# Kernel optimization log

Hardware: AMD Instinct MI355X
Metric: run time of the kernel (lower is better)

The kernel has to match this reference:

```python
import jax, jax.numpy as jnp
import numpy as np

COST_CLASS, COST_BBOX, COST_GIOU = 1.0, 5.0, 2.0


def box_cxcywh_to_xyxy(b):
    cx, cy, w, h = jnp.split(b, 4, axis=-1)
    return jnp.concatenate([cx - 0.5 * w, cy - 0.5 * h, cx + 0.5 * w, cy + 0.5 * h], axis=-1)


def generalized_box_iou(a, b):
    # a: [N,4], b: [T,4] in xyxy -> [N,T]
    area_a = (a[:, 2] - a[:, 0]) * (a[:, 3] - a[:, 1])
    area_b = (b[:, 2] - b[:, 0]) * (b[:, 3] - b[:, 1])
    lt = jnp.maximum(a[:, None, :2], b[None, :, :2])
    rb = jnp.minimum(a[:, None, 2:], b[None, :, 2:])
    wh = jnp.clip(rb - lt, 0.0)
    inter = wh[..., 0] * wh[..., 1]
    union = area_a[:, None] + area_b[None, :] - inter
    iou = inter / union
    lt_e = jnp.minimum(a[:, None, :2], b[None, :, :2])
    rb_e = jnp.maximum(a[:, None, 2:], b[None, :, 2:])
    wh_e = jnp.clip(rb_e - lt_e, 0.0)
    area_e = wh_e[..., 0] * wh_e[..., 1]
    return iou - (area_e - union) / area_e


def cost_matrix(pred_logits, pred_boxes, tgt_labels, tgt_boxes):
    B, Q, _ = pred_logits.shape
    probs = jax.nn.softmax(pred_logits.reshape(B * Q, -1), axis=-1)
    pb = pred_boxes.reshape(B * Q, 4)
    tl = tgt_labels.reshape(-1)
    tb = tgt_boxes.reshape(-1, 4)
    cc = -probs[:, tl]                                              # [BQ, BM]
    cb = jnp.sum(jnp.abs(pb[:, None, :] - tb[None, :, :]), axis=-1)  # L1 cdist
    cg = -generalized_box_iou(box_cxcywh_to_xyxy(pb), box_cxcywh_to_xyxy(tb))
    C = COST_CLASS * cc + COST_BBOX * cb + COST_GIOU * cg
    return C.reshape(B, Q, -1)


def hungarian(cost):
    # Jonker-Volgenant shortest-augmenting-path assignment.
    # cost: [n, m] with n <= m; returns the column assigned to each row, [n] int32.
    n, m = cost.shape
    INF = jnp.float32(1e30)

    def solve_row(i, uvp):
        u, v, p = uvp  # u:[n+1] row potentials (+dummy), v:[m+1], p:[m+1] row assigned per col
        p = p.at[m].set(i)  # virtual start column m holds the new row
        state = (jnp.int32(m), u, v, p,
                 jnp.full(m + 1, INF, jnp.float32),   # minv
                 jnp.zeros(m + 1, bool),              # used
                 jnp.zeros(m + 1, jnp.int32))         # way

        def cond(s):
            j0, _, _, p, _, _, _ = s
            return p[j0] != -1

        def body(s):
            j0, u, v, p, minv, used, way = s
            used = used.at[j0].set(True)
            i0 = p[j0]
            cur = jnp.where(used[:m], INF, cost[i0] - u[i0] - v[:m])
            better = cur < minv[:m]
            minv = minv.at[:m].set(jnp.where(better, cur, minv[:m]))
            way = way.at[:m].set(jnp.where(better, j0, way[:m]))
            masked = jnp.where(used[:m], INF, minv[:m])
            j1 = jnp.argmin(masked).astype(jnp.int32)
            delta = masked[j1]
            u = u.at[jnp.where(used, p, n)].add(jnp.where(used, delta, 0.0))
            v = jnp.where(used, v - delta, v)
            minv = jnp.where(used, minv, minv - delta)
            return (j1, u, v, p, minv, used, way)

        j0, u, v, p, minv, used, way = jax.lax.while_loop(cond, body, state)

        def a_cond(s):
            return s[0] != m

        def a_body(s):
            j0, p = s
            j1 = way[j0]
            return (j1, p.at[j0].set(p[j1]))

        _, p = jax.lax.while_loop(a_cond, a_body, (j0, p))
        return (u, v, p)

    u0 = jnp.zeros(n + 1, jnp.float32)
    v0 = jnp.zeros(m + 1, jnp.float32)
    p0 = jnp.full(m + 1, -1, jnp.int32)
    _, _, p = jax.lax.fori_loop(0, n, solve_row, (u0, v0, p0))
    row_of_col = p[:m]
    cols = jnp.arange(m, dtype=jnp.int32)
    col_of_row = jnp.zeros(n + 1, jnp.int32).at[
        jnp.where(row_of_col >= 0, row_of_col, n)].set(cols)
    return col_of_row[:n]


def setup_inputs() -> dict:
    key = jax.random.key(0)
    k1, k2, k3, k4 = jax.random.split(key, 4)
    B, Q, NCLS, M = 32, 300, 92, 50
    return {
        'pred_logits': jax.random.normal(k1, (B, Q, NCLS), jnp.float32),
        'pred_boxes': jax.random.uniform(k2, (B, Q, 4), dtype=jnp.float32),
        'tgt_labels': jax.random.randint(k3, (B, M), 0, NCLS),
        'tgt_boxes': jax.random.uniform(k4, (B, M, 4), dtype=jnp.float32),
    }


def reference(pred_logits, pred_boxes, tgt_labels, tgt_boxes):
    B, Q, _ = pred_logits.shape
    M = tgt_labels.shape[1]
    C = cost_matrix(pred_logits, pred_boxes, tgt_labels, tgt_boxes)  # [B, Q, B*M]
    # per-image block of columns: C[i, :, i*M:(i+1)*M]
    C4 = C.reshape(B, Q, B, M)
    C_per = jnp.transpose(jnp.diagonal(C4, axis1=0, axis2=2), (2, 0, 1))  # [B, Q, M]
    q = jax.vmap(hungarian)(jnp.transpose(C_per, (0, 2, 1)))  # [B, M]: query per target
    order = jnp.argsort(q, axis=1).astype(jnp.int32)
    pred_idx = jnp.take_along_axis(q, order, axis=1)  # sorted query indices
    gt_idx = order                                     # matching target indices
    return pred_idx, gt_idx, C
```

## Files before the change

kernel.cpp:

```cpp
#include <hip/hip_runtime.h>

#define NB   32
#define NQ   300
#define NCLS 92
#define NM   50
#define BM   (NB * NM)
#define BQ   (NB * NQ)
#define HM   NQ
#define HN   NM
#define PITCH 305
#define BIG  1e30f
#define HUNG_BLOCKS NB
#define COST_ROWS_PER_BLOCK 16
#define COST_BLOCKS (BQ / COST_ROWS_PER_BLOCK)
#define NBLOCKS (HUNG_BLOCKS + COST_BLOCKS)

typedef float vf4 __attribute__((ext_vector_type(4)));

#define FENCE() __threadfence_block()

#define DPP_XOR1  0xB1
#define DPP_XOR2  0x4E
#define DPP_HMIRR 0x141
#define DPP_MIRR  0x140
#define DPP_BC15  0x142
#define DPP_BC31  0x143

template <int C_>
__device__ __forceinline__ float dppk(float v) {
  return __int_as_float(__builtin_amdgcn_update_dpp(
      __float_as_int(v), __float_as_int(v), C_, 0xf, 0xf, false));
}
template <int C_>
__device__ __forceinline__ float dppz(float v) {
  return __int_as_float(
      __builtin_amdgcn_update_dpp(0, __float_as_int(v), C_, 0xf, 0xf, true));
}

__device__ __forceinline__ float rl63(float v) {
  return __int_as_float(__builtin_amdgcn_readlane(__float_as_int(v), 63));
}
__device__ __forceinline__ int rli(int v, int l) {
  return __builtin_amdgcn_readlane(v, l);
}
__device__ __forceinline__ float rlf(float v, int l) {
  return __int_as_float(__builtin_amdgcn_readlane(__float_as_int(v), l));
}

__device__ __forceinline__ float wredu_max(float v) {
  v = fmaxf(v, dppk<DPP_XOR1>(v));
  v = fmaxf(v, dppk<DPP_XOR2>(v));
  v = fmaxf(v, dppk<DPP_HMIRR>(v));
  v = fmaxf(v, dppk<DPP_MIRR>(v));
  v = fmaxf(v, dppk<DPP_BC15>(v));
  v = fmaxf(v, dppk<DPP_BC31>(v));
  return rl63(v);
}
__device__ __forceinline__ float wredu_min(float v) {
  v = fminf(v, dppk<DPP_XOR1>(v));
  v = fminf(v, dppk<DPP_XOR2>(v));
  v = fminf(v, dppk<DPP_HMIRR>(v));
  v = fminf(v, dppk<DPP_MIRR>(v));
  v = fminf(v, dppk<DPP_BC15>(v));
  v = fminf(v, dppk<DPP_BC31>(v));
  return rl63(v);
}
__device__ __forceinline__ float wredu_sum(float v) {
  v += dppz<DPP_XOR1>(v);
  v += dppz<DPP_XOR2>(v);
  v += dppz<DPP_HMIRR>(v);
  v += dppz<DPP_MIRR>(v);
  v += dppz<DPP_BC15>(v);
  v += dppz<DPP_BC31>(v);
  return rl63(v);
}

__device__ __forceinline__ float pair_cost(float ax1, float ay1, float ax2,
                                           float ay2, float areaA,
                                           const float4& pb, const float4& t,
                                           float negprob) {
  float cb = fabsf(pb.x - t.x) + fabsf(pb.y - t.y) +
             fabsf(pb.z - t.z) + fabsf(pb.w - t.w);
  float bx1 = t.x - 0.5f * t.z, by1 = t.y - 0.5f * t.w;
  float bx2 = t.x + 0.5f * t.z, by2 = t.y + 0.5f * t.w;
  float areaB = (bx2 - bx1) * (by2 - by1);
  float iw = fmaxf(fminf(ax2, bx2) - fmaxf(ax1, bx1), 0.f);
  float ih = fmaxf(fminf(ay2, by2) - fmaxf(ay1, by1), 0.f);
  float inter = iw * ih;
  float uni = areaA + areaB - inter;
  float iou = inter / uni;
  float ew = fmaxf(fmaxf(ax2, bx2) - fminf(ax1, bx1), 0.f);
  float eh = fmaxf(fmaxf(ay2, by2) - fminf(ay1, by1), 0.f);
  float areaE = ew * eh;
  float giou = iou - (areaE - uni) / areaE;
  return (negprob + 5.f * cb) - 2.f * giou;
}

__device__ __forceinline__ void wave_softmax(const float* __restrict__ lrow,
                                             float* prow, int lane) {
  float x0 = lrow[lane];
  float x1 = (lane + 64 < NCLS) ? lrow[lane + 64] : -BIG;
  float mx = wredu_max(fmaxf(x0, x1));
  float e0 = expf(x0 - mx), e1 = expf(x1 - mx);
  float s = wredu_sum(e0 + e1);
  prow[lane] = e0 / s;
  if (lane + 64 < NCLS) prow[lane + 64] = e1 / s;
  FENCE();
}

__global__ __launch_bounds__(1024) void fused_kernel(
    const float* __restrict__ logits, const float* __restrict__ pboxes,
    const int* __restrict__ tlab, const float* __restrict__ tbox,
    float* __restrict__ outp) {
  __shared__ float hc[HN * PITCH];
  __shared__ float probs_s[16][NCLS];
  __shared__ int   p[HM + 1];
  __shared__ int   way[HM];
  __shared__ int   qarr[HN];

  float* C = outp + 2 * BM;
  int tid = threadIdx.x, wave = tid >> 6, lane = tid & 63;

  if (blockIdx.x >= HUNG_BLOCKS) {
    int row = (blockIdx.x - HUNG_BLOCKS) * COST_ROWS_PER_BLOCK + wave;
    wave_softmax(logits + (size_t)row * NCLS, probs_s[wave], lane);

    float4 pb = reinterpret_cast<const float4*>(pboxes)[row];
    float ax1 = pb.x - 0.5f * pb.z, ay1 = pb.y - 0.5f * pb.w;
    float ax2 = pb.x + 0.5f * pb.z, ay2 = pb.y + 0.5f * pb.w;
    float areaA = (ax2 - ax1) * (ay2 - ay1);

    const float4* tbv = reinterpret_cast<const float4*>(tbox);
    const int4*   tlv = reinterpret_cast<const int4*>(tlab);
    vf4* crow = reinterpret_cast<vf4*>(C + (size_t)row * BM);
    for (int q4 = lane; q4 < BM / 4; q4 += 64) {
      int4 cls = tlv[q4];
      int clsa[4] = {cls.x, cls.y, cls.z, cls.w};
      vf4 o;
#pragma unroll
      for (int e = 0; e < 4; e++) {
        float4 t = tbv[q4 * 4 + e];
        o[e] = pair_cost(ax1, ay1, ax2, ay2, areaA, pb, t,
                         -probs_s[wave][clsa[e]]);
      }
      __builtin_nontemporal_store(o, &crow[q4]);
    }
    return;
  }

  int b = blockIdx.x;

  for (int x = tid; x <= HM; x += 1024) p[x] = -1;

  float4 t_reg = make_float4(0.f, 0.f, 0.f, 0.f);
  int cls_reg = 0;
  if (lane < NM) {
    t_reg = reinterpret_cast<const float4*>(tbox)[b * NM + lane];
    cls_reg = tlab[b * NM + lane];
  }

  const float4* pbv = reinterpret_cast<const float4*>(pboxes);
  for (int q = wave; q < NQ; q += 16) {
    const float* lrow = logits + (size_t)(b * NQ + q) * NCLS;
    float x0 = lrow[lane];
    float x1 = (lane + 64 < NCLS) ? lrow[lane + 64] : -BIG;
    float mx = wredu_max(fmaxf(x0, x1));
    float e0 = expf(x0 - mx), e1 = expf(x1 - mx);
    float s = wredu_sum(e0 + e1);
    float g0 = __shfl(x0, cls_reg, 64);
    float g1 = __shfl(x1, cls_reg, 64);
    float xsel = (cls_reg < 64) ? g0 : g1;
    float negp = -(expf(xsel - mx) / s);

    float4 pb = pbv[b * NQ + q];
    float ax1 = pb.x - 0.5f * pb.z, ay1 = pb.y - 0.5f * pb.w;
    float ax2 = pb.x + 0.5f * pb.z, ay2 = pb.y + 0.5f * pb.w;
    float areaA = (ax2 - ax1) * (ay2 - ay1);
    if (lane < NM) {
      hc[lane * PITCH + q] =
          pair_cost(ax1, ay1, ax2, ay2, areaA, pb, t_reg, negp);
    }
  }
  __syncthreads();
  if (wave != 0) return;


  float u_reg = 0.f;
  int am_reg = 0;
  if (lane < HN) {
    const float* r = &hc[lane * PITCH];
    float mn0 = BIG, mn1 = BIG;
    int a0 = 0, a1 = 1;
    for (int j = 0; j < HM; j += 2) {
      float va = r[j], vb = r[j + 1];
      if (va < mn0) { mn0 = va; a0 = j; }
      if (vb < mn1) { mn1 = vb; a1 = j + 1; }
    }
    bool takeOdd = (mn1 < mn0) || (mn1 == mn0 && a1 < a0);
    u_reg = takeOdd ? mn1 : mn0;
    am_reg = takeOdd ? a1 : a0;
  }

  unsigned amask = 0;
  unsigned long long pending = 0;
  for (int i = 0; i < HN; i++) {
    int jm = rli(am_reg, i);
    unsigned mrem = (unsigned)rli((int)amask, jm & 63);
    if (!((mrem >> (jm >> 6)) & 1u)) {
      if (lane == (jm & 63)) amask |= 1u << (jm >> 6);
      if (lane == 0) p[jm] = i;
    } else {
      pending |= 1ull << i;
    }
  }
  FENCE();

  float v_r[5], minv_r[5];
#pragma unroll
  for (int k = 0; k < 5; k++) v_r[k] = 0.f;

  while (pending) {
    int i_start = (int)__ffsll((long long)pending) - 1;
    pending &= pending - 1;
#pragma unroll
    for (int k = 0; k < 5; k++) minv_r[k] = BIG;
    unsigned usedc = 0;
    unsigned long long used_rows = 1ull << i_start;
    int i0 = i_start, j0 = HM, jfree = -1;
    float ui0 = rlf(u_reg, i0);

    while (true) {
      float best = BIG; int bj = 0;
      const float* hrow = &hc[i0 * PITCH];
#pragma unroll
      for (int k = 0; k < 5; k++) {
        int j = lane + 64 * k;
        if (j < HM && !((usedc >> k) & 1u)) {
          float cur = hrow[j] - ui0 - v_r[k];
          if (cur < minv_r[k]) { minv_r[k] = cur; way[j] = j0; }
          if (minv_r[k] < best) { best = minv_r[k]; bj = j; }
        }
      }
      float wmin = wredu_min(best);
      unsigned long long ball = __ballot(best == wmin);
      int src = (int)__ffsll((long long)ball) - 1;
      int j1 = rli(bj, src);
      float delta = wmin;

      int psel = p[j1];

      if ((used_rows >> lane) & 1ull) u_reg += delta;
#pragma unroll
      for (int k = 0; k < 5; k++) {
        int j = lane + 64 * k;
        if (j < HM) {
          if ((usedc >> k) & 1u) v_r[k] -= delta;
          else                   minv_r[k] -= delta;
        }
      }
      if (lane == (j1 & 63)) usedc |= 1u << (j1 >> 6);

      if (psel == -1) { jfree = j1; break; }
      i0 = psel;
      used_rows |= 1ull << i0;
      ui0 = rlf(u_reg, i0);
      j0 = j1;
    }

    int jj = jfree;
    while (jj != HM) {
      int jn = way[jj];
      int pv = (jn == HM) ? i_start : p[jn];
      p[jj] = pv;
      jj = jn;
    }
    FENCE();
  }

  for (int j = lane; j < HM; j += 64) {
    int r = p[j];
    if (r >= 0) qarr[r] = j;
  }
  FENCE();
  if (lane < HN) {
    int qi = qarr[lane];
    int rank = 0;
    for (int t = 0; t < HN; t++) rank += (qarr[t] < qi);
    outp[(size_t)b * NM + rank] = (float)qi;
    outp[BM + (size_t)b * NM + rank] = (float)lane;
  }
}

extern "C" void kernel_launch(void* const* d_in, const int* in_sizes, int n_in,
                              void* d_out, int out_size, void* d_ws, size_t ws_size,
                              hipStream_t stream) {
  const float* logits = (const float*)d_in[0];
  const float* pboxes = (const float*)d_in[1];
  const int*   tlab   = (const int*)d_in[2];
  const float* tbox   = (const float*)d_in[3];
  float* out = (float*)d_out;

  fused_kernel<<<dim3(NBLOCKS), dim3(1024), 0, stream>>>(
      logits, pboxes, tlab, tbox, out);
}
```

Baseline: 117.4 us.

## Keep Hungarian assignment and path arrays in registers, prefetch next cost row

Moves the Hungarian solver's p[] and way[] arrays out of shared memory into per-lane registers, accessed with readlane and lane-predicated writes. The next cost row is prefetched into registers as soon as the matched row is known. The per-lane argmin becomes a branchless tree. Divisions are replaced with hardware reciprocal, the wave gets raised scheduling priority, and small unroll and launch-bound tweaks are added. This targets LDS latency on the serial augmenting-path critical path, at the cost of more VGPRs, readlane select chains, and slightly less exact reciprocal arithmetic.

```diff
diff --git a/kernel.cpp b/kernel.cpp
--- a/kernel.cpp
+++ b/kernel.cpp
@@ -46,6 +46,9 @@
 __device__ __forceinline__ float rlf(float v, int l) {
   return __int_as_float(__builtin_amdgcn_readlane(__float_as_int(v), l));
 }
+__device__ __forceinline__ float frcp(float x) {
+  return __builtin_amdgcn_rcpf(x);
+}
 
 __device__ __forceinline__ float wredu_max(float v) {
   v = fmaxf(v, dppk<DPP_XOR1>(v));
@@ -74,6 +77,25 @@
   v += dppz<DPP_BC31>(v);
   return rl63(v);
 }
+
+#define RLSEL(dst, kk, ll, a0, a1, a2, a3, a4)        \
+  {                                                   \
+    if ((kk) == 0)      dst = rli((a0), (ll));        \
+    else if ((kk) == 1) dst = rli((a1), (ll));        \
+    else if ((kk) == 2) dst = rli((a2), (ll));        \
+    else if ((kk) == 3) dst = rli((a3), (ll));        \
+    else                dst = rli((a4), (ll));        \
+  }
+#define WRSEL(kk, ll, val, a0, a1, a2, a3, a4)        \
+  {                                                   \
+    if (lane == (ll)) {                               \
+      if ((kk) == 0)      a0 = (val);                 \
+      else if ((kk) == 1) a1 = (val);                 \
+      else if ((kk) == 2) a2 = (val);                 \
+      else if ((kk) == 3) a3 = (val);                 \
+      else                a4 = (val);                 \
+    }                                                 \
+  }
 
 __device__ __forceinline__ float pair_cost(float ax1, float ay1, float ax2,
                                            float ay2, float areaA,
@@ -88,11 +110,11 @@
   float ih = fmaxf(fminf(ay2, by2) - fmaxf(ay1, by1), 0.f);
   float inter = iw * ih;
   float uni = areaA + areaB - inter;
-  float iou = inter / uni;
+  float iou = inter * frcp(uni);
   float ew = fmaxf(fmaxf(ax2, bx2) - fminf(ax1, bx1), 0.f);
   float eh = fmaxf(fmaxf(ay2, by2) - fminf(ay1, by1), 0.f);
   float areaE = ew * eh;
-  float giou = iou - (areaE - uni) / areaE;
+  float giou = iou - (areaE - uni) * frcp(areaE);
   return (negprob + 5.f * cb) - 2.f * giou;
 }
 
@@ -103,19 +125,17 @@
   float mx = wredu_max(fmaxf(x0, x1));
   float e0 = expf(x0 - mx), e1 = expf(x1 - mx);
   float s = wredu_sum(e0 + e1);
-  prow[lane] = e0 / s;
-  if (lane + 64 < NCLS) prow[lane + 64] = e1 / s;
-  FENCE();
-}
-
-__global__ __launch_bounds__(1024) void fused_kernel(
+  float rs = frcp(s);
+  prow[lane] = e0 * rs;
+  if (lane + 64 < NCLS) prow[lane + 64] = e1 * rs;
+}
+
+__global__ __launch_bounds__(1024, 8) void fused_kernel(
     const float* __restrict__ logits, const float* __restrict__ pboxes,
     const int* __restrict__ tlab, const float* __restrict__ tbox,
     float* __restrict__ outp) {
   __shared__ float hc[HN * PITCH];
   __shared__ float probs_s[16][NCLS];
-  __shared__ int   p[HM + 1];
-  __shared__ int   way[HM];
   __shared__ int   qarr[HN];
 
   float* C = outp + 2 * BM;
@@ -133,6 +153,7 @@
     const float4* tbv = reinterpret_cast<const float4*>(tbox);
     const int4*   tlv = reinterpret_cast<const int4*>(tlab);
     vf4* crow = reinterpret_cast<vf4*>(C + (size_t)row * BM);
+#pragma unroll 2
     for (int q4 = lane; q4 < BM / 4; q4 += 64) {
       int4 cls = tlv[q4];
       int clsa[4] = {cls.x, cls.y, cls.z, cls.w};
@@ -149,8 +170,6 @@
   }
 
   int b = blockIdx.x;
-
-  for (int x = tid; x <= HM; x += 1024) p[x] = -1;
 
   float4 t_reg = make_float4(0.f, 0.f, 0.f, 0.f);
   int cls_reg = 0;
@@ -160,6 +179,7 @@
   }
 
   const float4* pbv = reinterpret_cast<const float4*>(pboxes);
+#pragma unroll 2
   for (int q = wave; q < NQ; q += 16) {
     const float* lrow = logits + (size_t)(b * NQ + q) * NCLS;
     float x0 = lrow[lane];
@@ -170,7 +190,7 @@
     float g0 = __shfl(x0, cls_reg, 64);
     float g1 = __shfl(x1, cls_reg, 64);
     float xsel = (cls_reg < 64) ? g0 : g1;
-    float negp = -(expf(xsel - mx) / s);
+    float negp = -(expf(xsel - mx) * frcp(s));
 
     float4 pb = pbv[b * NQ + q];
     float ax1 = pb.x - 0.5f * pb.z, ay1 = pb.y - 0.5f * pb.w;
@@ -183,6 +203,8 @@
   }
   __syncthreads();
   if (wave != 0) return;
+
+  __builtin_amdgcn_s_setprio(1);
 
 
   float u_reg = 0.f;
@@ -201,6 +223,9 @@
     am_reg = takeOdd ? a1 : a0;
   }
 
+  int pr0 = -1, pr1 = -1, pr2 = -1, pr3 = -1, pr4 = -1;
+  int wy0 = 0, wy1 = 0, wy2 = 0, wy3 = 0, wy4 = 0;
+
   unsigned amask = 0;
   unsigned long long pending = 0;
   for (int i = 0; i < HN; i++) {
@@ -208,14 +233,14 @@
     unsigned mrem = (unsigned)rli((int)amask, jm & 63);
     if (!((mrem >> (jm >> 6)) & 1u)) {
       if (lane == (jm & 63)) amask |= 1u << (jm >> 6);
-      if (lane == 0) p[jm] = i;
+      int kk = jm >> 6, ll = jm & 63;
+      WRSEL(kk, ll, i, pr0, pr1, pr2, pr3, pr4);
     } else {
       pending |= 1ull << i;
     }
   }
-  FENCE();
-
-  float v_r[5], minv_r[5];
+
+  float v_r[5], minv_r[5], h[5];
 #pragma unroll
   for (int k = 0; k < 5; k++) v_r[k] = 0.f;
 
@@ -229,25 +254,55 @@
     int i0 = i_start, j0 = HM, jfree = -1;
     float ui0 = rlf(u_reg, i0);
 
+#pragma unroll
+    for (int k = 0; k < 5; k++) {
+      int j = lane + 64 * k;
+      h[k] = (j < HM) ? hc[i0 * PITCH + j] : BIG;
+    }
+
     while (true) {
-      float best = BIG; int bj = 0;
-      const float* hrow = &hc[i0 * PITCH];
+      float bk[5];
 #pragma unroll
       for (int k = 0; k < 5; k++) {
         int j = lane + 64 * k;
-        if (j < HM && !((usedc >> k) & 1u)) {
-          float cur = hrow[j] - ui0 - v_r[k];
-          if (cur < minv_r[k]) { minv_r[k] = cur; way[j] = j0; }
-          if (minv_r[k] < best) { best = minv_r[k]; bj = j; }
+        bool act = (j < HM) && !((usedc >> k) & 1u);
+        float cur = h[k] - ui0 - v_r[k];
+        if (act && cur < minv_r[k]) {
+          minv_r[k] = cur;
+          if (k == 0) wy0 = j0; else if (k == 1) wy1 = j0;
+          else if (k == 2) wy2 = j0; else if (k == 3) wy3 = j0;
+          else wy4 = j0;
         }
-      }
+        bk[k] = act ? minv_r[k] : BIG;
+      }
+      float m01 = (bk[1] < bk[0]) ? bk[1] : bk[0];
+      int   j01 = (bk[1] < bk[0]) ? lane + 64 : lane;
+      float m23 = (bk[3] < bk[2]) ? bk[3] : bk[2];
+      int   j23 = (bk[3] < bk[2]) ? lane + 192 : lane + 128;
+      float m03 = (m23 < m01) ? m23 : m01;
+      int   j03 = (m23 < m01) ? j23 : j01;
+      float best = (bk[4] < m03) ? bk[4] : m03;
+      int   bj   = (bk[4] < m03) ? lane + 256 : j03;
+
       float wmin = wredu_min(best);
       unsigned long long ball = __ballot(best == wmin);
       int src = (int)__ffsll((long long)ball) - 1;
       int j1 = rli(bj, src);
       float delta = wmin;
 
-      int psel = p[j1];
+      int psel;
+      {
+        int kk = j1 >> 6, ll = j1 & 63;
+        RLSEL(psel, kk, ll, pr0, pr1, pr2, pr3, pr4);
+      }
+
+      if (psel != -1) {
+#pragma unroll
+        for (int k = 0; k < 5; k++) {
+          int j = lane + 64 * k;
+          h[k] = (j < HM) ? hc[psel * PITCH + j] : BIG;
+        }
+      }
 
       if ((used_rows >> lane) & 1ull) u_reg += delta;
 #pragma unroll
@@ -269,17 +324,28 @@
 
     int jj = jfree;
     while (jj != HM) {
-      int jn = way[jj];
-      int pv = (jn == HM) ? i_start : p[jn];
-      p[jj] = pv;
+      int kk = jj >> 6, ll = jj & 63;
+      int jn;
+      RLSEL(jn, kk, ll, wy0, wy1, wy2, wy3, wy4);
+      int pv;
+      if (jn == HM) {
+        pv = i_start;
+      } else {
+        int k2 = jn >> 6, l2 = jn & 63;
+        RLSEL(pv, k2, l2, pr0, pr1, pr2, pr3, pr4);
+      }
+      WRSEL(kk, ll, pv, pr0, pr1, pr2, pr3, pr4);
       jj = jn;
     }
-    FENCE();
-  }
-
-  for (int j = lane; j < HM; j += 64) {
-    int r = p[j];
-    if (r >= 0) qarr[r] = j;
+  }
+
+  {
+    int j, r;
+    j = lane;       r = pr0; if (r >= 0) qarr[r] = j;
+    j = lane + 64;  r = pr1; if (r >= 0) qarr[r] = j;
+    j = lane + 128; r = pr2; if (r >= 0) qarr[r] = j;
+    j = lane + 192; r = pr3; if (r >= 0) qarr[r] = j;
+    j = lane + 256; r = pr4; if (j < HM && r >= 0) qarr[r] = j;
   }
   FENCE();
   if (lane < HN) {
```

Result: slower. 122.1 us (+4.0%).
